# Performance work log

Measured on AMD Instinct MI355X. Metric: run time of the kernel, lower is better.

## Reference

```python
import jax, jax.numpy as jnp
import numpy as np

BATCH, SEQ_LEN, NOISE_DIM, SEQ_DIM, HID = 8192, 256, 8, 4, 64

def setup_inputs() -> dict:
    key = jax.random.key(0)
    ks = jax.random.split(key, 6)
    s = lambda k, shp, fan: jax.random.normal(k, shp, jnp.float32) * (1.0 / np.sqrt(fan))
    return {
        "noise": jax.random.normal(ks[0], (BATCH, SEQ_LEN, NOISE_DIM), jnp.float32),
        "Wx": s(ks[1], (SEQ_DIM + NOISE_DIM, 4 * HID), SEQ_DIM + NOISE_DIM),
        "Wh": s(ks[2], (HID, 4 * HID), HID),
        "b": jnp.zeros((4 * HID,), jnp.float32),
        "W1": s(ks[3], (HID, HID), HID), "b1": jnp.zeros((HID,), jnp.float32),
        "W2": s(ks[4], (HID, HID), HID), "b2": jnp.zeros((HID,), jnp.float32),
        "W3": s(ks[5], (HID, SEQ_DIM), HID), "b3": jnp.zeros((SEQ_DIM,), jnp.float32),
    }

def reference(noise, Wx, Wh, b, W1, b1, W2, b2, W3, b3):
    batch = noise.shape[0]
    # log_series=True -> initial x is zeros
    x0 = jnp.zeros((batch, SEQ_DIM), noise.dtype)
    h0 = jnp.zeros((batch, HID), noise.dtype)
    c0 = jnp.zeros((batch, HID), noise.dtype)
    noise_t = jnp.swapaxes(noise[:, : SEQ_LEN - 1, :], 0, 1)  # [L-1, B, noise_dim]

    def step(carry, n_t):
        x, h, c = carry
        inp = jnp.concatenate([x, n_t], axis=-1)           # [B, seq_dim+noise_dim]
        z = inp @ Wx + h @ Wh + b                          # [B, 4H], keras gate order i,f,g,o
        i, f, g, o = jnp.split(z, 4, axis=-1)
        c = jax.nn.sigmoid(f) * c + jax.nn.sigmoid(i) * jnp.tanh(g)
        h = jax.nn.sigmoid(o) * jnp.tanh(c)
        y = jax.nn.relu(h @ W1 + b1)
        y = jax.nn.relu(y @ W2 + b2)
        x_new = y @ W3 + b3                                # [B, seq_dim]
        return (x_new, h, c), x_new

    _, xs = jax.lax.scan(step, (x0, h0, c0), noise_t)       # [L-1, B, seq_dim]
    seq = jnp.concatenate([x0[None], xs], axis=0)           # [L, B, seq_dim]
    seq = jnp.swapaxes(seq, 0, 1)                           # [B, L, seq_dim]
    return jnp.cumsum(seq, axis=1)
```

## Files before the change

kernel.cpp:

```cpp
#include <hip/hip_runtime.h>


typedef _Float16 h8 __attribute__((ext_vector_type(8)));
typedef __fp16 p2h __attribute__((ext_vector_type(2)));
typedef float f4 __attribute__((ext_vector_type(4)));

#define MFMA(a, b, c) __builtin_amdgcn_mfma_f32_16x16x32_f16(a, b, c, 0, 0, 0)

constexpr int SEQ = 256, STEPS = 255, ND = 8, SD = 4, HID = 64, G4 = 256;
constexpr int HST  = 72;
constexpr int A2ST = 24;

__device__ __forceinline__ void store4h(_Float16* p, f4 v) {
    p2h lo = __builtin_amdgcn_cvt_pkrtz(v[0], v[1]);
    p2h hi = __builtin_amdgcn_cvt_pkrtz(v[2], v[3]);
    float2 st;
    st.x = __builtin_bit_cast(float, lo);
    st.y = __builtin_bit_cast(float, hi);
    *(float2*)p = st;
}
__device__ __forceinline__ void store2h(_Float16* p, float a, float b_) {
    p2h v = __builtin_amdgcn_cvt_pkrtz(a, b_);
    *(float*)p = __builtin_bit_cast(float, v);
}

__global__ __launch_bounds__(256, 2) void genlstm_kernel(
    const float* __restrict__ noise, const float* __restrict__ Wx,
    const float* __restrict__ Wh, const float* __restrict__ b,
    const float* __restrict__ W1, const float* __restrict__ b1,
    const float* __restrict__ W2, const float* __restrict__ b2,
    const float* __restrict__ W3, const float* __restrict__ b3,
    float* __restrict__ out)
{
    __shared__ alignas(16) _Float16 Hb[2 * 16 * HST];
    __shared__ alignas(16) _Float16 Y1b[16 * HST];
    __shared__ alignas(16) _Float16 Y2b[16 * HST];
    __shared__ alignas(16) _Float16 A2b[4 * 16 * A2ST];
    __shared__ alignas(16) _Float16 Zb[8];

    const int tid = threadIdx.x, wid = tid >> 6, lane = tid & 63;
    const int col = lane & 15, quad = lane >> 4, q8 = quad * 8;
    const int row0 = blockIdx.x * 16;
    const int n0 = wid * 16 + col;
    const int wq = wid * 16 + quad * 4;

    h8 wg[4][3], w1f[2], w2f[2], w3f[2];
    #pragma unroll
    for (int g = 0; g < 4; ++g)
        #pragma unroll
        for (int s = 0; s < 3; ++s)
            #pragma unroll
            for (int j = 0; j < 8; ++j) {
                const int k = 32 * s + q8 + j;
                const int n = 64 * g + n0;
                float v;
                if (k < 64) v = Wh[k * G4 + n];
                else if (k < 76) v = Wx[(k - 64) * G4 + n];
                else v = 0.0f;
                wg[g][s][j] = (_Float16)v;
            }
    #pragma unroll
    for (int s = 0; s < 2; ++s)
        #pragma unroll
        for (int j = 0; j < 8; ++j) {
            const int k = 32 * s + q8 + j;
            w1f[s][j] = (_Float16)W1[k * HID + n0];
            w2f[s][j] = (_Float16)W2[k * HID + n0];
            w3f[s][j] = (_Float16)(col < 4 ? W3[k * SD + col] : 0.0f);
        }
    f4 bzv[4], b1v, b2v, b3v;
    #pragma unroll
    for (int r = 0; r < 4; ++r) {
        #pragma unroll
        for (int g = 0; g < 4; ++g) bzv[g][r] = b[64 * g + wq + r];
        b1v[r] = b1[wq + r];
        b2v[r] = b2[wq + r];
        b3v[r] = (quad == 0) ? b3[r] : 0.0f;
    }

    for (int i = tid; i < 2 * 16 * HST; i += 256) Hb[i] = (_Float16)0;
    for (int i = tid; i < 4 * 16 * A2ST; i += 256) A2b[i] = (_Float16)0;
    if (tid < 8) Zb[tid] = (_Float16)0;
    if (tid < 16) {
        float4 z; z.x = z.y = z.z = z.w = 0.0f;
        *(float4*)(out + (size_t)(row0 + tid) * SEQ * SD) = z;
    }
    __syncthreads();

    const int nrow = lane >> 2, ncc = (lane & 3) * 2;
    const float* nptr = noise + ((size_t)(row0 + nrow) * SEQ) * ND + ncc;
    _Float16* a2n = &A2b[(wid * 16 + nrow) * A2ST + 4 + ncc];
    _Float16* a2x = &A2b[(wid * 16 + col) * A2ST];
    const _Float16* a2rd = (quad < 2) ? &A2b[(wid * 16 + col) * A2ST + 8 * quad] : Zb;
    _Float16* Hrow[2] = { &Hb[col * HST], &Hb[(16 + col) * HST] };
    _Float16* Y1row = &Y1b[col * HST];
    _Float16* Y2row = &Y2b[col * HST];
    float* outp = out + ((size_t)(row0 + col) * SEQ + 1) * SD;

    {
        float2 nz = *(const float2*)nptr;
        store2h(a2n, nz.x, nz.y);
        nptr += ND;
    }

    f4 cst = {0.f, 0.f, 0.f, 0.f}, run = {0.f, 0.f, 0.f, 0.f};
    f4 zi = bzv[0], zf = bzv[1], zg = bzv[2], zo = bzv[3];
    h8 h0, h1;

    auto body = [&](int pb) {
        float2 nz = *(const float2*)nptr;
        nptr += ND;

        h8 a2 = *(const h8*)a2rd;
        zi = MFMA(wg[0][2], a2, zi);
        zf = MFMA(wg[1][2], a2, zf);
        zg = MFMA(wg[2][2], a2, zg);
        zo = MFMA(wg[3][2], a2, zo);

        f4 hv;
        #pragma unroll
        for (int r = 0; r < 4; ++r) {
            float Ei = __expf(-fmaxf(zi[r], -15.f));
            float Ef = __expf(-fmaxf(zf[r], -15.f));
            float Eg = __expf(-2.f * fmaxf(zg[r], -15.f));
            float Eo = __expf(-zo[r]);
            float Di = 1.f + Ei, Df = 1.f + Ef, Dg = 1.f + Eg, Do = 1.f + Eo;
            float DiDg = Di * Dg;
            float cn = (cst[r] * DiDg + (2.f - Dg) * Df) *
                       __builtin_amdgcn_rcpf(Df * DiDg);
            cst[r] = cn;
            float Ec = __expf(-2.f * fmaxf(cn, -15.f));
            hv[r] = (1.f - Ec) * __builtin_amdgcn_rcpf(Do * (1.f + Ec));
        }
        store4h(Hrow[pb ^ 1] + wq, hv);
        __syncthreads();

        const _Float16* hb = Hrow[pb ^ 1];
        h0 = *(const h8*)(hb + q8);
        h1 = *(const h8*)(hb + 32 + q8);
        f4 y1 = b1v;
        y1 = MFMA(w1f[0], h0, y1);
        y1 = MFMA(w1f[1], h1, y1);
        #pragma unroll
        for (int r = 0; r < 4; ++r) y1[r] = fmaxf(y1[r], 0.0f);
        store4h(Y1row + wq, y1);
        __syncthreads();

        h8 p0 = *(const h8*)(Y1row + q8);
        h8 p1 = *(const h8*)(Y1row + 32 + q8);
        f4 y2 = b2v;
        y2 = MFMA(w2f[0], p0, y2);
        y2 = MFMA(w2f[1], p1, y2);
        #pragma unroll
        for (int r = 0; r < 4; ++r) y2[r] = fmaxf(y2[r], 0.0f);
        store4h(Y2row + wq, y2);
        __syncthreads();

        h8 q0 = *(const h8*)(Y2row + q8);
        h8 q1 = *(const h8*)(Y2row + 32 + q8);
        f4 x = b3v;
        x = MFMA(w3f[0], q0, x);
        x = MFMA(w3f[1], q1, x);

        zi = bzv[0]; zi = MFMA(wg[0][0], h0, zi); zi = MFMA(wg[0][1], h1, zi);
        zf = bzv[1]; zf = MFMA(wg[1][0], h0, zf); zf = MFMA(wg[1][1], h1, zf);
        zg = bzv[2]; zg = MFMA(wg[2][0], h0, zg); zg = MFMA(wg[2][1], h1, zg);
        zo = bzv[3]; zo = MFMA(wg[3][0], h0, zo); zo = MFMA(wg[3][1], h1, zo);

        if (quad == 0) {
            store4h(a2x, x);
            if (wid == 0) {
                run += x;
                *(f4*)outp = run;
            }
        }
        store2h(a2n, nz.x, nz.y);
        outp += SD;
    };

    #pragma unroll 1
    for (int t = 0; t < STEPS - 1; t += 2) {
        body(0);
        body(1);
    }
    body(0);
}

extern "C" void kernel_launch(void* const* d_in, const int* in_sizes, int n_in,
                              void* d_out, int out_size, void* d_ws, size_t ws_size,
                              hipStream_t stream) {
    genlstm_kernel<<<512, 256, 0, stream>>>(
        (const float*)d_in[0], (const float*)d_in[1], (const float*)d_in[2],
        (const float*)d_in[3], (const float*)d_in[4], (const float*)d_in[5],
        (const float*)d_in[6], (const float*)d_in[7], (const float*)d_in[8],
        (const float*)d_in[9], (float*)d_out);
}
```

Before: 405.3 us.

## Compute the MLP redundantly per wave to drop per-step block barriers

```diff
diff --git a/kernel.cpp b/kernel.cpp
--- a/kernel.cpp
+++ b/kernel.cpp
@@ -8,8 +8,7 @@
 #define MFMA(a, b, c) __builtin_amdgcn_mfma_f32_16x16x32_f16(a, b, c, 0, 0, 0)
 
 constexpr int SEQ = 256, STEPS = 255, ND = 8, SD = 4, HID = 64, G4 = 256;
-constexpr int HST  = 72;
-constexpr int A2ST = 24;
+constexpr int HST = 72;
 
 __device__ __forceinline__ void store4h(_Float16* p, f4 v) {
     p2h lo = __builtin_amdgcn_cvt_pkrtz(v[0], v[1]);
@@ -18,10 +17,6 @@
     st.x = __builtin_bit_cast(float, lo);
     st.y = __builtin_bit_cast(float, hi);
     *(float2*)p = st;
-}
-__device__ __forceinline__ void store2h(_Float16* p, float a, float b_) {
-    p2h v = __builtin_amdgcn_cvt_pkrtz(a, b_);
-    *(float*)p = __builtin_bit_cast(float, v);
 }
 
 __global__ __launch_bounds__(256, 2) void genlstm_kernel(
@@ -33,10 +28,7 @@
     float* __restrict__ out)
 {
     __shared__ alignas(16) _Float16 Hb[2 * 16 * HST];
-    __shared__ alignas(16) _Float16 Y1b[16 * HST];
-    __shared__ alignas(16) _Float16 Y2b[16 * HST];
-    __shared__ alignas(16) _Float16 A2b[4 * 16 * A2ST];
-    __shared__ alignas(16) _Float16 Zb[8];
+    __shared__ alignas(16) _Float16 Yp[4 * 16 * HST];
 
     const int tid = threadIdx.x, wid = tid >> 6, lane = tid & 63;
     const int col = lane & 15, quad = lane >> 4, q8 = quad * 8;
@@ -44,7 +36,7 @@
     const int n0 = wid * 16 + col;
     const int wq = wid * 16 + quad * 4;
 
-    h8 wg[4][3], w1f[2], w2f[2], w3f[2];
+    h8 wg[4][3];
     #pragma unroll
     for (int g = 0; g < 4; ++g)
         #pragma unroll
@@ -56,66 +48,79 @@
                 float v;
                 if (k < 64) v = Wh[k * G4 + n];
                 else if (k < 76) v = Wx[(k - 64) * G4 + n];
+                else if (k == 76) v = b[n];
                 else v = 0.0f;
                 wg[g][s][j] = (_Float16)v;
             }
+    h8 w1f[4][2], w2f[4][2], w3f[2];
+    #pragma unroll
+    for (int tn = 0; tn < 4; ++tn)
+        #pragma unroll
+        for (int s = 0; s < 2; ++s)
+            #pragma unroll
+            for (int j = 0; j < 8; ++j) {
+                const int k = 32 * s + q8 + j;
+                w1f[tn][s][j] = (_Float16)W1[k * HID + 16 * tn + col];
+                w2f[tn][s][j] = (_Float16)W2[k * HID + 16 * tn + col];
+            }
     #pragma unroll
     for (int s = 0; s < 2; ++s)
         #pragma unroll
         for (int j = 0; j < 8; ++j) {
             const int k = 32 * s + q8 + j;
-            w1f[s][j] = (_Float16)W1[k * HID + n0];
-            w2f[s][j] = (_Float16)W2[k * HID + n0];
             w3f[s][j] = (_Float16)(col < 4 ? W3[k * SD + col] : 0.0f);
         }
-    f4 bzv[4], b1v, b2v, b3v;
+    f4 b1v[4], b2v[4], b3v;
     #pragma unroll
     for (int r = 0; r < 4; ++r) {
         #pragma unroll
-        for (int g = 0; g < 4; ++g) bzv[g][r] = b[64 * g + wq + r];
-        b1v[r] = b1[wq + r];
-        b2v[r] = b2[wq + r];
+        for (int tn = 0; tn < 4; ++tn) {
+            b1v[tn][r] = b1[16 * tn + quad * 4 + r];
+            b2v[tn][r] = b2[16 * tn + quad * 4 + r];
+        }
         b3v[r] = (quad == 0) ? b3[r] : 0.0f;
     }
 
-    for (int i = tid; i < 2 * 16 * HST; i += 256) Hb[i] = (_Float16)0;
-    for (int i = tid; i < 4 * 16 * A2ST; i += 256) A2b[i] = (_Float16)0;
-    if (tid < 8) Zb[tid] = (_Float16)0;
     if (tid < 16) {
         float4 z; z.x = z.y = z.z = z.w = 0.0f;
         *(float4*)(out + (size_t)(row0 + tid) * SEQ * SD) = z;
     }
-    __syncthreads();
-
-    const int nrow = lane >> 2, ncc = (lane & 3) * 2;
-    const float* nptr = noise + ((size_t)(row0 + nrow) * SEQ) * ND + ncc;
-    _Float16* a2n = &A2b[(wid * 16 + nrow) * A2ST + 4 + ncc];
-    _Float16* a2x = &A2b[(wid * 16 + col) * A2ST];
-    const _Float16* a2rd = (quad < 2) ? &A2b[(wid * 16 + col) * A2ST + 8 * quad] : Zb;
+
+    const float* nptr = noise + (size_t)(row0 + col) * SEQ * ND + (quad & 1) * 4;
+    float4 nf = {0.f, 0.f, 0.f, 0.f};
+    if (quad < 2) nf = *(const float4*)nptr;
+    nptr += ND;
+
     _Float16* Hrow[2] = { &Hb[col * HST], &Hb[(16 + col) * HST] };
-    _Float16* Y1row = &Y1b[col * HST];
-    _Float16* Y2row = &Y2b[col * HST];
+    _Float16* Yr = &Yp[(wid * 16 + col) * HST];
     float* outp = out + ((size_t)(row0 + col) * SEQ + 1) * SD;
 
-    {
-        float2 nz = *(const float2*)nptr;
-        store2h(a2n, nz.x, nz.y);
+    const f4 fz = {0.f, 0.f, 0.f, 0.f};
+    f4 cst = fz, run = fz, xv = fz;
+    f4 zi = fz, zf = fz, zg = fz, zo = fz;
+    h8 h0, h1;
+
+    auto body = [&](int pb) {
+        union { h8 v; p2h p[4]; } a2;
+        p2h zz = __builtin_amdgcn_cvt_pkrtz(0.f, 0.f);
+        a2.p[0] = a2.p[1] = a2.p[2] = a2.p[3] = zz;
+        if (quad == 0) {
+            a2.p[0] = __builtin_amdgcn_cvt_pkrtz(xv[0], xv[1]);
+            a2.p[1] = __builtin_amdgcn_cvt_pkrtz(xv[2], xv[3]);
+            a2.p[2] = __builtin_amdgcn_cvt_pkrtz(nf.x, nf.y);
+            a2.p[3] = __builtin_amdgcn_cvt_pkrtz(nf.z, nf.w);
+        } else if (quad == 1) {
+            a2.p[0] = __builtin_amdgcn_cvt_pkrtz(nf.x, nf.y);
+            a2.p[1] = __builtin_amdgcn_cvt_pkrtz(nf.z, nf.w);
+            a2.p[2] = __builtin_amdgcn_cvt_pkrtz(1.0f, 0.f);
+        }
+        zi = MFMA(wg[0][2], a2.v, zi);
+        zf = MFMA(wg[1][2], a2.v, zf);
+        zg = MFMA(wg[2][2], a2.v, zg);
+        zo = MFMA(wg[3][2], a2.v, zo);
+
+        if (quad < 2) nf = *(const float4*)nptr;
         nptr += ND;
-    }
-
-    f4 cst = {0.f, 0.f, 0.f, 0.f}, run = {0.f, 0.f, 0.f, 0.f};
-    f4 zi = bzv[0], zf = bzv[1], zg = bzv[2], zo = bzv[3];
-    h8 h0, h1;
-
-    auto body = [&](int pb) {
-        float2 nz = *(const float2*)nptr;
-        nptr += ND;
-
-        h8 a2 = *(const h8*)a2rd;
-        zi = MFMA(wg[0][2], a2, zi);
-        zf = MFMA(wg[1][2], a2, zf);
-        zg = MFMA(wg[2][2], a2, zg);
-        zo = MFMA(wg[3][2], a2, zo);
 
         f4 hv;
         #pragma unroll
@@ -138,43 +143,44 @@
         const _Float16* hb = Hrow[pb ^ 1];
         h0 = *(const h8*)(hb + q8);
         h1 = *(const h8*)(hb + 32 + q8);
-        f4 y1 = b1v;
-        y1 = MFMA(w1f[0], h0, y1);
-        y1 = MFMA(w1f[1], h1, y1);
-        #pragma unroll
-        for (int r = 0; r < 4; ++r) y1[r] = fmaxf(y1[r], 0.0f);
-        store4h(Y1row + wq, y1);
-        __syncthreads();
-
-        h8 p0 = *(const h8*)(Y1row + q8);
-        h8 p1 = *(const h8*)(Y1row + 32 + q8);
-        f4 y2 = b2v;
-        y2 = MFMA(w2f[0], p0, y2);
-        y2 = MFMA(w2f[1], p1, y2);
-        #pragma unroll
-        for (int r = 0; r < 4; ++r) y2[r] = fmaxf(y2[r], 0.0f);
-        store4h(Y2row + wq, y2);
-        __syncthreads();
-
-        h8 q0 = *(const h8*)(Y2row + q8);
-        h8 q1 = *(const h8*)(Y2row + 32 + q8);
-        f4 x = b3v;
-        x = MFMA(w3f[0], q0, x);
-        x = MFMA(w3f[1], q1, x);
-
-        zi = bzv[0]; zi = MFMA(wg[0][0], h0, zi); zi = MFMA(wg[0][1], h1, zi);
-        zf = bzv[1]; zf = MFMA(wg[1][0], h0, zf); zf = MFMA(wg[1][1], h1, zf);
-        zg = bzv[2]; zg = MFMA(wg[2][0], h0, zg); zg = MFMA(wg[2][1], h1, zg);
-        zo = bzv[3]; zo = MFMA(wg[3][0], h0, zo); zo = MFMA(wg[3][1], h1, zo);
-
-        if (quad == 0) {
-            store4h(a2x, x);
-            if (wid == 0) {
-                run += x;
-                *(f4*)outp = run;
-            }
-        }
-        store2h(a2n, nz.x, nz.y);
+
+        #pragma unroll
+        for (int tn = 0; tn < 4; ++tn) {
+            f4 a = b1v[tn];
+            a = MFMA(w1f[tn][0], h0, a);
+            a = MFMA(w1f[tn][1], h1, a);
+            #pragma unroll
+            for (int r = 0; r < 4; ++r) a[r] = fmaxf(a[r], 0.f);
+            store4h(Yr + 16 * tn + 4 * quad, a);
+        }
+
+        zi = fz; zi = MFMA(wg[0][0], h0, zi); zi = MFMA(wg[0][1], h1, zi);
+        zf = fz; zf = MFMA(wg[1][0], h0, zf); zf = MFMA(wg[1][1], h1, zf);
+        zg = fz; zg = MFMA(wg[2][0], h0, zg); zg = MFMA(wg[2][1], h1, zg);
+        zo = fz; zo = MFMA(wg[3][0], h0, zo); zo = MFMA(wg[3][1], h1, zo);
+
+        h8 p0 = *(const h8*)(Yr + q8);
+        h8 p1 = *(const h8*)(Yr + 32 + q8);
+        #pragma unroll
+        for (int tn = 0; tn < 4; ++tn) {
+            f4 a = b2v[tn];
+            a = MFMA(w2f[tn][0], p0, a);
+            a = MFMA(w2f[tn][1], p1, a);
+            #pragma unroll
+            for (int r = 0; r < 4; ++r) a[r] = fmaxf(a[r], 0.f);
+            store4h(Yr + 16 * tn + 4 * quad, a);
+        }
+
+        h8 q0 = *(const h8*)(Yr + q8);
+        h8 q1 = *(const h8*)(Yr + 32 + q8);
+        xv = b3v;
+        xv = MFMA(w3f[0], q0, xv);
+        xv = MFMA(w3f[1], q1, xv);
+
+        if (wid == 0 && quad == 0) {
+            run += xv;
+            *(f4*)outp = run;
+        }
         outp += SD;
     };
 
```

Result: slower. 503.0 us (+24.1%).

## Process two independent 16-row batch groups per block to interleave recurrences

Applied to the files above, without the earlier changes.

```diff
diff --git a/kernel.cpp b/kernel.cpp
--- a/kernel.cpp
+++ b/kernel.cpp
@@ -24,7 +24,7 @@
     *(float*)p = __builtin_bit_cast(float, v);
 }
 
-__global__ __launch_bounds__(256, 2) void genlstm_kernel(
+__global__ __launch_bounds__(256, 1) void genlstm_kernel(
     const float* __restrict__ noise, const float* __restrict__ Wx,
     const float* __restrict__ Wh, const float* __restrict__ b,
     const float* __restrict__ W1, const float* __restrict__ b1,
@@ -32,19 +32,19 @@
     const float* __restrict__ W3, const float* __restrict__ b3,
     float* __restrict__ out)
 {
-    __shared__ alignas(16) _Float16 Hb[2 * 16 * HST];
-    __shared__ alignas(16) _Float16 Y1b[16 * HST];
-    __shared__ alignas(16) _Float16 Y2b[16 * HST];
-    __shared__ alignas(16) _Float16 A2b[4 * 16 * A2ST];
+    __shared__ alignas(16) _Float16 Hb[2][2 * 16 * HST];
+    __shared__ alignas(16) _Float16 Y1b[2][16 * HST];
+    __shared__ alignas(16) _Float16 Y2b[2][16 * HST];
+    __shared__ alignas(16) _Float16 A2b[2][4 * 16 * A2ST];
     __shared__ alignas(16) _Float16 Zb[8];
 
     const int tid = threadIdx.x, wid = tid >> 6, lane = tid & 63;
     const int col = lane & 15, quad = lane >> 4, q8 = quad * 8;
-    const int row0 = blockIdx.x * 16;
+    const int row0 = blockIdx.x * 32;
     const int n0 = wid * 16 + col;
     const int wq = wid * 16 + quad * 4;
 
-    h8 wg[4][3], w1f[2], w2f[2], w3f[2];
+    h8 wg[4][3];
     #pragma unroll
     for (int g = 0; g < 4; ++g)
         #pragma unroll
@@ -56,9 +56,11 @@
                 float v;
                 if (k < 64) v = Wh[k * G4 + n];
                 else if (k < 76) v = Wx[(k - 64) * G4 + n];
+                else if (k == 76) v = b[n];
                 else v = 0.0f;
                 wg[g][s][j] = (_Float16)v;
             }
+    h8 w1f[2], w2f[2], w3f[2];
     #pragma unroll
     for (int s = 0; s < 2; ++s)
         #pragma unroll
@@ -68,114 +70,142 @@
             w2f[s][j] = (_Float16)W2[k * HID + n0];
             w3f[s][j] = (_Float16)(col < 4 ? W3[k * SD + col] : 0.0f);
         }
-    f4 bzv[4], b1v, b2v, b3v;
+    f4 b1v, b2v, b3v;
     #pragma unroll
     for (int r = 0; r < 4; ++r) {
-        #pragma unroll
-        for (int g = 0; g < 4; ++g) bzv[g][r] = b[64 * g + wq + r];
         b1v[r] = b1[wq + r];
         b2v[r] = b2[wq + r];
         b3v[r] = (quad == 0) ? b3[r] : 0.0f;
     }
 
-    for (int i = tid; i < 2 * 16 * HST; i += 256) Hb[i] = (_Float16)0;
-    for (int i = tid; i < 4 * 16 * A2ST; i += 256) A2b[i] = (_Float16)0;
+    for (int i = tid; i < 2 * 2 * 16 * HST; i += 256) (&Hb[0][0])[i] = (_Float16)0;
+    for (int i = tid; i < 2 * 4 * 16 * A2ST; i += 256)
+        (&A2b[0][0])[i] = (i % A2ST == 12) ? (_Float16)1 : (_Float16)0;
     if (tid < 8) Zb[tid] = (_Float16)0;
-    if (tid < 16) {
+    if (tid < 32) {
         float4 z; z.x = z.y = z.z = z.w = 0.0f;
         *(float4*)(out + (size_t)(row0 + tid) * SEQ * SD) = z;
     }
     __syncthreads();
 
     const int nrow = lane >> 2, ncc = (lane & 3) * 2;
-    const float* nptr = noise + ((size_t)(row0 + nrow) * SEQ) * ND + ncc;
-    _Float16* a2n = &A2b[(wid * 16 + nrow) * A2ST + 4 + ncc];
-    _Float16* a2x = &A2b[(wid * 16 + col) * A2ST];
-    const _Float16* a2rd = (quad < 2) ? &A2b[(wid * 16 + col) * A2ST + 8 * quad] : Zb;
-    _Float16* Hrow[2] = { &Hb[col * HST], &Hb[(16 + col) * HST] };
-    _Float16* Y1row = &Y1b[col * HST];
-    _Float16* Y2row = &Y2b[col * HST];
-    float* outp = out + ((size_t)(row0 + col) * SEQ + 1) * SD;
-
-    {
-        float2 nz = *(const float2*)nptr;
-        store2h(a2n, nz.x, nz.y);
-        nptr += ND;
-    }
-
-    f4 cst = {0.f, 0.f, 0.f, 0.f}, run = {0.f, 0.f, 0.f, 0.f};
-    f4 zi = bzv[0], zf = bzv[1], zg = bzv[2], zo = bzv[3];
-    h8 h0, h1;
+    const float* nptr[2];
+    _Float16* a2n_[2];
+    _Float16* a2x_[2];
+    const _Float16* a2rd_[2];
+    _Float16* Y1r_[2];
+    _Float16* Y2r_[2];
+    float* outp_[2];
+    #pragma unroll
+    for (int g = 0; g < 2; ++g) {
+        nptr[g]  = noise + ((size_t)(row0 + 16 * g + nrow) * SEQ) * ND + ncc;
+        a2n_[g]  = &A2b[g][(wid * 16 + nrow) * A2ST + 4 + ncc];
+        a2x_[g]  = &A2b[g][(wid * 16 + col) * A2ST];
+        a2rd_[g] = (quad < 2) ? &A2b[g][(wid * 16 + col) * A2ST + 8 * quad] : Zb;
+        Y1r_[g]  = &Y1b[g][col * HST];
+        Y2r_[g]  = &Y2b[g][col * HST];
+        outp_[g] = out + ((size_t)(row0 + 16 * g + col) * SEQ + 1) * SD;
+    }
+
+    #pragma unroll
+    for (int g = 0; g < 2; ++g) {
+        float2 nz = *(const float2*)nptr[g];
+        store2h(a2n_[g], nz.x, nz.y);
+        nptr[g] += ND;
+    }
+
+    const f4 fz = {0.f, 0.f, 0.f, 0.f};
+    f4 cst[2] = {fz, fz}, run[2] = {fz, fz};
+    f4 zi[2] = {fz, fz}, zf[2] = {fz, fz}, zg[2] = {fz, fz}, zo[2] = {fz, fz};
+    h8 h0[2], h1[2];
 
     auto body = [&](int pb) {
-        float2 nz = *(const float2*)nptr;
-        nptr += ND;
-
-        h8 a2 = *(const h8*)a2rd;
-        zi = MFMA(wg[0][2], a2, zi);
-        zf = MFMA(wg[1][2], a2, zf);
-        zg = MFMA(wg[2][2], a2, zg);
-        zo = MFMA(wg[3][2], a2, zo);
-
-        f4 hv;
-        #pragma unroll
-        for (int r = 0; r < 4; ++r) {
-            float Ei = __expf(-fmaxf(zi[r], -15.f));
-            float Ef = __expf(-fmaxf(zf[r], -15.f));
-            float Eg = __expf(-2.f * fmaxf(zg[r], -15.f));
-            float Eo = __expf(-zo[r]);
-            float Di = 1.f + Ei, Df = 1.f + Ef, Dg = 1.f + Eg, Do = 1.f + Eo;
-            float DiDg = Di * Dg;
-            float cn = (cst[r] * DiDg + (2.f - Dg) * Df) *
-                       __builtin_amdgcn_rcpf(Df * DiDg);
-            cst[r] = cn;
-            float Ec = __expf(-2.f * fmaxf(cn, -15.f));
-            hv[r] = (1.f - Ec) * __builtin_amdgcn_rcpf(Do * (1.f + Ec));
-        }
-        store4h(Hrow[pb ^ 1] + wq, hv);
+        float2 nz[2];
+        #pragma unroll
+        for (int g = 0; g < 2; ++g) {
+            nz[g] = *(const float2*)nptr[g];
+            nptr[g] += ND;
+            h8 a2 = *(const h8*)a2rd_[g];
+            zi[g] = MFMA(wg[0][2], a2, zi[g]);
+            zf[g] = MFMA(wg[1][2], a2, zf[g]);
+            zg[g] = MFMA(wg[2][2], a2, zg[g]);
+            zo[g] = MFMA(wg[3][2], a2, zo[g]);
+        }
+
+        #pragma unroll
+        for (int g = 0; g < 2; ++g) {
+            f4 hv;
+            #pragma unroll
+            for (int r = 0; r < 4; ++r) {
+                float Ei = __expf(-fmaxf(zi[g][r], -15.f));
+                float Ef = __expf(-fmaxf(zf[g][r], -15.f));
+                float Eg = __expf(-2.f * fmaxf(zg[g][r], -15.f));
+                float Eo = __expf(-zo[g][r]);
+                float Di = 1.f + Ei, Df = 1.f + Ef, Dg = 1.f + Eg, Do = 1.f + Eo;
+                float DiDg = Di * Dg;
+                float cn = (cst[g][r] * DiDg + (2.f - Dg) * Df) *
+                           __builtin_amdgcn_rcpf(Df * DiDg);
+                cst[g][r] = cn;
+                float Ec = __expf(-2.f * fmaxf(cn, -15.f));
+                hv[r] = (1.f - Ec) * __builtin_amdgcn_rcpf(Do * (1.f + Ec));
+            }
+            store4h(&Hb[g][((pb ^ 1) * 16 + col) * HST] + wq, hv);
+        }
         __syncthreads();
 
-        const _Float16* hb = Hrow[pb ^ 1];
-        h0 = *(const h8*)(hb + q8);
-        h1 = *(const h8*)(hb + 32 + q8);
-        f4 y1 = b1v;
-        y1 = MFMA(w1f[0], h0, y1);
-        y1 = MFMA(w1f[1], h1, y1);
-        #pragma unroll
-        for (int r = 0; r < 4; ++r) y1[r] = fmaxf(y1[r], 0.0f);
-        store4h(Y1row + wq, y1);
+        #pragma unroll
+        for (int g = 0; g < 2; ++g) {
+            const _Float16* hb = &Hb[g][((pb ^ 1) * 16 + col) * HST];
+            h0[g] = *(const h8*)(hb + q8);
+            h1[g] = *(const h8*)(hb + 32 + q8);
+            f4 y1 = b1v;
+            y1 = MFMA(w1f[0], h0[g], y1);
+            y1 = MFMA(w1f[1], h1[g], y1);
+            #pragma unroll
+            for (int r = 0; r < 4; ++r) y1[r] = fmaxf(y1[r], 0.0f);
+            store4h(Y1r_[g] + wq, y1);
+        }
+
+        #pragma unroll
+        for (int g = 0; g < 2; ++g) {
+            zi[g] = fz; zi[g] = MFMA(wg[0][0], h0[g], zi[g]); zi[g] = MFMA(wg[0][1], h1[g], zi[g]);
+            zf[g] = fz; zf[g] = MFMA(wg[1][0], h0[g], zf[g]); zf[g] = MFMA(wg[1][1], h1[g], zf[g]);
+            zg[g] = fz; zg[g] = MFMA(wg[2][0], h0[g], zg[g]); zg[g] = MFMA(wg[2][1], h1[g], zg[g]);
+            zo[g] = fz; zo[g] = MFMA(wg[3][0], h0[g], zo[g]); zo[g] = MFMA(wg[3][1], h1[g], zo[g]);
+        }
         __syncthreads();
 
-        h8 p0 = *(const h8*)(Y1row + q8);
-        h8 p1 = *(const h8*)(Y1row + 32 + q8);
-        f4 y2 = b2v;
-        y2 = MFMA(w2f[0], p0, y2);
-        y2 = MFMA(w2f[1], p1, y2);
-        #pragma unroll
-        for (int r = 0; r < 4; ++r) y2[r] = fmaxf(y2[r], 0.0f);
-        store4h(Y2row + wq, y2);
+        #pragma unroll
+        for (int g = 0; g < 2; ++g) {
+            h8 p0 = *(const h8*)(Y1r_[g] + q8);
+            h8 p1 = *(const h8*)(Y1r_[g] + 32 + q8);
+            f4 y2 = b2v;
+            y2 = MFMA(w2f[0], p0, y2);
+            y2 = MFMA(w2f[1], p1, y2);
+            #pragma unroll
+            for (int r = 0; r < 4; ++r) y2[r] = fmaxf(y2[r], 0.0f);
+            store4h(Y2r_[g] + wq, y2);
+        }
         __syncthreads();
 
-        h8 q0 = *(const h8*)(Y2row + q8);
-        h8 q1 = *(const h8*)(Y2row + 32 + q8);
-        f4 x = b3v;
-        x = MFMA(w3f[0], q0, x);
-        x = MFMA(w3f[1], q1, x);
-
-        zi = bzv[0]; zi = MFMA(wg[0][0], h0, zi); zi = MFMA(wg[0][1], h1, zi);
-        zf = bzv[1]; zf = MFMA(wg[1][0], h0, zf); zf = MFMA(wg[1][1], h1, zf);
-        zg = bzv[2]; zg = MFMA(wg[2][0], h0, zg); zg = MFMA(wg[2][1], h1, zg);
-        zo = bzv[3]; zo = MFMA(wg[3][0], h0, zo); zo = MFMA(wg[3][1], h1, zo);
-
-        if (quad == 0) {
-            store4h(a2x, x);
-            if (wid == 0) {
-                run += x;
-                *(f4*)outp = run;
+        #pragma unroll
+        for (int g = 0; g < 2; ++g) {
+            h8 q0 = *(const h8*)(Y2r_[g] + q8);
+            h8 q1 = *(const h8*)(Y2r_[g] + 32 + q8);
+            f4 x = b3v;
+            x = MFMA(w3f[0], q0, x);
+            x = MFMA(w3f[1], q1, x);
+
+            if (quad == 0) {
+                store4h(a2x_[g], x);
+                if (wid == 0) {
+                    run[g] += x;
+                    *(f4*)outp_[g] = run[g];
+                }
             }
-        }
-        store2h(a2n, nz.x, nz.y);
-        outp += SD;
+            store2h(a2n_[g], nz[g].x, nz[g].y);
+            outp_[g] += SD;
+        }
     };
 
     #pragma unroll 1
@@ -189,7 +219,7 @@
 extern "C" void kernel_launch(void* const* d_in, const int* in_sizes, int n_in,
                               void* d_out, int out_size, void* d_ws, size_t ws_size,
                               hipStream_t stream) {
-    genlstm_kernel<<<512, 256, 0, stream>>>(
+    genlstm_kernel<<<256, 256, 0, stream>>>(
         (const float*)d_in[0], (const float*)d_in[1], (const float*)d_in[2],
         (const float*)d_in[3], (const float*)d_in[4], (const float*)d_in[5],
         (const float*)d_in[6], (const float*)d_in[7], (const float*)d_in[8],
```

Result: slower. 537.9 us (+32.7%).

## Fold W3 into Wx gate weights and feed noise straight from registers

Applied to the files above, without the earlier changes.

```diff
diff --git a/kernel.cpp b/kernel.cpp
--- a/kernel.cpp
+++ b/kernel.cpp
@@ -6,10 +6,11 @@
 typedef float f4 __attribute__((ext_vector_type(4)));
 
 #define MFMA(a, b, c) __builtin_amdgcn_mfma_f32_16x16x32_f16(a, b, c, 0, 0, 0)
+#define EXP2(x) __builtin_amdgcn_exp2f(x)
 
 constexpr int SEQ = 256, STEPS = 255, ND = 8, SD = 4, HID = 64, G4 = 256;
-constexpr int HST  = 72;
-constexpr int A2ST = 24;
+constexpr int HST = 72;
+constexpr float LOG2E = 1.44269504f;
 
 __device__ __forceinline__ void store4h(_Float16* p, f4 v) {
     p2h lo = __builtin_amdgcn_cvt_pkrtz(v[0], v[1]);
@@ -19,10 +20,6 @@
     st.y = __builtin_bit_cast(float, hi);
     *(float2*)p = st;
 }
-__device__ __forceinline__ void store2h(_Float16* p, float a, float b_) {
-    p2h v = __builtin_amdgcn_cvt_pkrtz(a, b_);
-    *(float*)p = __builtin_bit_cast(float, v);
-}
 
 __global__ __launch_bounds__(256, 2) void genlstm_kernel(
     const float* __restrict__ noise, const float* __restrict__ Wx,
@@ -32,11 +29,9 @@
     const float* __restrict__ W3, const float* __restrict__ b3,
     float* __restrict__ out)
 {
-    __shared__ alignas(16) _Float16 Hb[2 * 16 * HST];
+    __shared__ alignas(16) _Float16 Hb[16 * HST];
     __shared__ alignas(16) _Float16 Y1b[16 * HST];
     __shared__ alignas(16) _Float16 Y2b[16 * HST];
-    __shared__ alignas(16) _Float16 A2b[4 * 16 * A2ST];
-    __shared__ alignas(16) _Float16 Zb[8];
 
     const int tid = threadIdx.x, wid = tid >> 6, lane = tid & 63;
     const int col = lane & 15, quad = lane >> 4, q8 = quad * 8;
@@ -44,21 +39,38 @@
     const int n0 = wid * 16 + col;
     const int wq = wid * 16 + quad * 4;
 
-    h8 wg[4][3], w1f[2], w2f[2], w3f[2];
+    const float gsc[4] = {LOG2E, LOG2E, 2.f * LOG2E, LOG2E};
+
+    h8 wg[4][3];
     #pragma unroll
     for (int g = 0; g < 4; ++g)
         #pragma unroll
         for (int s = 0; s < 3; ++s)
             #pragma unroll
             for (int j = 0; j < 8; ++j) {
-                const int k = 32 * s + q8 + j;
                 const int n = 64 * g + n0;
                 float v;
-                if (k < 64) v = Wh[k * G4 + n];
-                else if (k < 76) v = Wx[(k - 64) * G4 + n];
-                else v = 0.0f;
-                wg[g][s][j] = (_Float16)v;
+                if (s < 2) v = Wh[(32 * s + q8 + j) * G4 + n];
+                else       v = (q8 + j < 8) ? Wx[(4 + q8 + j) * G4 + n] : 0.0f;
+                wg[g][s][j] = (_Float16)(v * gsc[g]);
             }
+    h8 wgy[4][2];
+    #pragma unroll
+    for (int s = 0; s < 2; ++s)
+        #pragma unroll
+        for (int j = 0; j < 8; ++j) {
+            const int k = 32 * s + q8 + j;
+            const float w30 = W3[k * SD + 0], w31 = W3[k * SD + 1];
+            const float w32 = W3[k * SD + 2], w33 = W3[k * SD + 3];
+            #pragma unroll
+            for (int g = 0; g < 4; ++g) {
+                const int n = 64 * g + n0;
+                float acc = w30 * Wx[0 * G4 + n] + w31 * Wx[1 * G4 + n] +
+                            w32 * Wx[2 * G4 + n] + w33 * Wx[3 * G4 + n];
+                wgy[g][s][j] = (_Float16)(acc * gsc[g]);
+            }
+        }
+    h8 w1f[2], w2f[2], w3f[2];
     #pragma unroll
     for (int s = 0; s < 2; ++s)
         #pragma unroll
@@ -68,122 +80,130 @@
             w2f[s][j] = (_Float16)W2[k * HID + n0];
             w3f[s][j] = (_Float16)(col < 4 ? W3[k * SD + col] : 0.0f);
         }
-    f4 bzv[4], b1v, b2v, b3v;
+    f4 bzv[4], bz0[4], b1v, b2v, b3v;
     #pragma unroll
     for (int r = 0; r < 4; ++r) {
         #pragma unroll
-        for (int g = 0; g < 4; ++g) bzv[g][r] = b[64 * g + wq + r];
+        for (int g = 0; g < 4; ++g) {
+            const int n = 64 * g + wq + r;
+            float bx = b3[0] * Wx[0 * G4 + n] + b3[1] * Wx[1 * G4 + n] +
+                       b3[2] * Wx[2 * G4 + n] + b3[3] * Wx[3 * G4 + n];
+            bz0[g][r] = b[n] * gsc[g];
+            bzv[g][r] = (b[n] + bx) * gsc[g];
+        }
         b1v[r] = b1[wq + r];
         b2v[r] = b2[wq + r];
         b3v[r] = (quad == 0) ? b3[r] : 0.0f;
     }
 
-    for (int i = tid; i < 2 * 16 * HST; i += 256) Hb[i] = (_Float16)0;
-    for (int i = tid; i < 4 * 16 * A2ST; i += 256) A2b[i] = (_Float16)0;
-    if (tid < 8) Zb[tid] = (_Float16)0;
     if (tid < 16) {
         float4 z; z.x = z.y = z.z = z.w = 0.0f;
         *(float4*)(out + (size_t)(row0 + tid) * SEQ * SD) = z;
     }
-    __syncthreads();
-
-    const int nrow = lane >> 2, ncc = (lane & 3) * 2;
-    const float* nptr = noise + ((size_t)(row0 + nrow) * SEQ) * ND + ncc;
-    _Float16* a2n = &A2b[(wid * 16 + nrow) * A2ST + 4 + ncc];
-    _Float16* a2x = &A2b[(wid * 16 + col) * A2ST];
-    const _Float16* a2rd = (quad < 2) ? &A2b[(wid * 16 + col) * A2ST + 8 * quad] : Zb;
-    _Float16* Hrow[2] = { &Hb[col * HST], &Hb[(16 + col) * HST] };
+
+    _Float16* Hrow = &Hb[col * HST];
     _Float16* Y1row = &Y1b[col * HST];
     _Float16* Y2row = &Y2b[col * HST];
     float* outp = out + ((size_t)(row0 + col) * SEQ + 1) * SD;
 
+    const float* npt = noise + (size_t)(row0 + col) * SEQ * ND;
+    const float4 fz4 = {0.f, 0.f, 0.f, 0.f};
+    const f4 fz = {0.f, 0.f, 0.f, 0.f};
+
+    f4 cst = fz, run = fz;
+    f4 zi, zf, zg, zo;
+
     {
-        float2 nz = *(const float2*)nptr;
-        store2h(a2n, nz.x, nz.y);
-        nptr += ND;
-    }
-
-    f4 cst = {0.f, 0.f, 0.f, 0.f}, run = {0.f, 0.f, 0.f, 0.f};
-    f4 zi = bzv[0], zf = bzv[1], zg = bzv[2], zo = bzv[3];
-    h8 h0, h1;
-
-    auto body = [&](int pb) {
-        float2 nz = *(const float2*)nptr;
-        nptr += ND;
-
-        h8 a2 = *(const h8*)a2rd;
-        zi = MFMA(wg[0][2], a2, zi);
-        zf = MFMA(wg[1][2], a2, zf);
-        zg = MFMA(wg[2][2], a2, zg);
-        zo = MFMA(wg[3][2], a2, zo);
+        float4 nf0 = fz4, nf1 = fz4;
+        if (quad == 0) { nf0 = *(const float4*)npt; nf1 = *(const float4*)(npt + 4); }
+        npt += ND;
+        union { h8 v; p2h p[4]; } nb;
+        nb.p[0] = __builtin_amdgcn_cvt_pkrtz(nf0.x, nf0.y);
+        nb.p[1] = __builtin_amdgcn_cvt_pkrtz(nf0.z, nf0.w);
+        nb.p[2] = __builtin_amdgcn_cvt_pkrtz(nf1.x, nf1.y);
+        nb.p[3] = __builtin_amdgcn_cvt_pkrtz(nf1.z, nf1.w);
+        zi = MFMA(wg[0][2], nb.v, bz0[0]);
+        zf = MFMA(wg[1][2], nb.v, bz0[1]);
+        zg = MFMA(wg[2][2], nb.v, bz0[2]);
+        zo = MFMA(wg[3][2], nb.v, bz0[3]);
+    }
+
+    #pragma unroll 1
+    for (int t = 0; t < STEPS; ++t) {
+        float4 nf0 = fz4, nf1 = fz4;
+        if (quad == 0) { nf0 = *(const float4*)npt; nf1 = *(const float4*)(npt + 4); }
+        npt += ND;
 
         f4 hv;
         #pragma unroll
         for (int r = 0; r < 4; ++r) {
-            float Ei = __expf(-fmaxf(zi[r], -15.f));
-            float Ef = __expf(-fmaxf(zf[r], -15.f));
-            float Eg = __expf(-2.f * fmaxf(zg[r], -15.f));
-            float Eo = __expf(-zo[r]);
+            float Ei = EXP2(-fmaxf(zi[r], -15.f * LOG2E));
+            float Ef = EXP2(-fmaxf(zf[r], -15.f * LOG2E));
+            float Eg = EXP2(-fmaxf(zg[r], -30.f * LOG2E));
+            float Eo = EXP2(-zo[r]);
             float Di = 1.f + Ei, Df = 1.f + Ef, Dg = 1.f + Eg, Do = 1.f + Eo;
             float DiDg = Di * Dg;
             float cn = (cst[r] * DiDg + (2.f - Dg) * Df) *
                        __builtin_amdgcn_rcpf(Df * DiDg);
             cst[r] = cn;
-            float Ec = __expf(-2.f * fmaxf(cn, -15.f));
+            float Ec = EXP2(fmaxf(cn, -15.f) * (-2.f * LOG2E));
             hv[r] = (1.f - Ec) * __builtin_amdgcn_rcpf(Do * (1.f + Ec));
         }
-        store4h(Hrow[pb ^ 1] + wq, hv);
+        store4h(Hrow + wq, hv);
         __syncthreads();
 
-        const _Float16* hb = Hrow[pb ^ 1];
-        h0 = *(const h8*)(hb + q8);
-        h1 = *(const h8*)(hb + 32 + q8);
-        f4 y1 = b1v;
-        y1 = MFMA(w1f[0], h0, y1);
+        h8 h0 = *(const h8*)(&Hb[col * HST] + q8);
+        h8 h1 = *(const h8*)(&Hb[col * HST] + 32 + q8);
+
+        f4 y1 = MFMA(w1f[0], h0, b1v);
         y1 = MFMA(w1f[1], h1, y1);
         #pragma unroll
-        for (int r = 0; r < 4; ++r) y1[r] = fmaxf(y1[r], 0.0f);
+        for (int r = 0; r < 4; ++r) y1[r] = fmaxf(y1[r], 0.f);
         store4h(Y1row + wq, y1);
+
+        zi = MFMA(wg[0][0], h0, bzv[0]); zi = MFMA(wg[0][1], h1, zi);
+        zf = MFMA(wg[1][0], h0, bzv[1]); zf = MFMA(wg[1][1], h1, zf);
+        zg = MFMA(wg[2][0], h0, bzv[2]); zg = MFMA(wg[2][1], h1, zg);
+        zo = MFMA(wg[3][0], h0, bzv[3]); zo = MFMA(wg[3][1], h1, zo);
         __syncthreads();
 
         h8 p0 = *(const h8*)(Y1row + q8);
         h8 p1 = *(const h8*)(Y1row + 32 + q8);
-        f4 y2 = b2v;
-        y2 = MFMA(w2f[0], p0, y2);
+        f4 y2 = MFMA(w2f[0], p0, b2v);
         y2 = MFMA(w2f[1], p1, y2);
         #pragma unroll
-        for (int r = 0; r < 4; ++r) y2[r] = fmaxf(y2[r], 0.0f);
+        for (int r = 0; r < 4; ++r) y2[r] = fmaxf(y2[r], 0.f);
         store4h(Y2row + wq, y2);
         __syncthreads();
 
         h8 q0 = *(const h8*)(Y2row + q8);
         h8 q1 = *(const h8*)(Y2row + 32 + q8);
-        f4 x = b3v;
-        x = MFMA(w3f[0], q0, x);
-        x = MFMA(w3f[1], q1, x);
-
-        zi = bzv[0]; zi = MFMA(wg[0][0], h0, zi); zi = MFMA(wg[0][1], h1, zi);
-        zf = bzv[1]; zf = MFMA(wg[1][0], h0, zf); zf = MFMA(wg[1][1], h1, zf);
-        zg = bzv[2]; zg = MFMA(wg[2][0], h0, zg); zg = MFMA(wg[2][1], h1, zg);
-        zo = bzv[3]; zo = MFMA(wg[3][0], h0, zo); zo = MFMA(wg[3][1], h1, zo);
-
-        if (quad == 0) {
-            store4h(a2x, x);
-            if (wid == 0) {
+
+        zi = MFMA(wgy[0][0], q0, zi); zi = MFMA(wgy[0][1], q1, zi);
+        zf = MFMA(wgy[1][0], q0, zf); zf = MFMA(wgy[1][1], q1, zf);
+        zg = MFMA(wgy[2][0], q0, zg); zg = MFMA(wgy[2][1], q1, zg);
+        zo = MFMA(wgy[3][0], q0, zo); zo = MFMA(wgy[3][1], q1, zo);
+
+        union { h8 v; p2h p[4]; } nb;
+        nb.p[0] = __builtin_amdgcn_cvt_pkrtz(nf0.x, nf0.y);
+        nb.p[1] = __builtin_amdgcn_cvt_pkrtz(nf0.z, nf0.w);
+        nb.p[2] = __builtin_amdgcn_cvt_pkrtz(nf1.x, nf1.y);
+        nb.p[3] = __builtin_amdgcn_cvt_pkrtz(nf1.z, nf1.w);
+        zi = MFMA(wg[0][2], nb.v, zi);
+        zf = MFMA(wg[1][2], nb.v, zf);
+        zg = MFMA(wg[2][2], nb.v, zg);
+        zo = MFMA(wg[3][2], nb.v, zo);
+
+        if (wid == 0) {
+            f4 x = MFMA(w3f[0], q0, b3v);
+            x = MFMA(w3f[1], q1, x);
+            if (quad == 0) {
                 run += x;
                 *(f4*)outp = run;
             }
         }
-        store2h(a2n, nz.x, nz.y);
         outp += SD;
-    };
-
-    #pragma unroll 1
-    for (int t = 0; t < STEPS - 1; t += 2) {
-        body(0);
-        body(1);
-    }
-    body(0);
+    }
 }
 
 extern "C" void kernel_launch(void* const* d_in, const int* in_sizes, int n_in,
```

Measured after the change: 436.7 us. 1.08x slower.
